# Kernel tuning notes

Hardware: AMD Instinct MI355X
Metric: run time of the kernel (lower is better)

Reference implementation:

```python
import jax, jax.numpy as jnp
import numpy as np

# OHEM CE constants (match init_kwargs)
THRESH = -np.log(0.7).astype(np.float32)  # threshold stored as -log(p)
N_MIN = 262144                            # B*H*W // 16
IGNORE_INDEX = 255


def setup_inputs() -> dict:
    key = jax.random.key(0)
    k1, k2 = jax.random.split(key)
    B, C, H, W = 16, 19, 512, 512
    inp = jax.random.normal(k1, (B, C, H, W), dtype=jnp.float32)
    target = jax.random.randint(k2, (B, H, W), 0, C, dtype=jnp.int64)
    k3 = jax.random.fold_in(key, 7)
    ign = jax.random.uniform(k3, (B, H, W)) < 0.02
    target = jnp.where(ign, jnp.asarray(IGNORE_INDEX, jnp.int64), target)
    return {"input": inp, "target": target}


def reference(input, target):
    # per-pixel cross entropy with ignore_index, reduction='none'
    logp = jax.nn.log_softmax(input, axis=1)              # (B,C,H,W)
    valid = target != IGNORE_INDEX                        # (B,H,W)
    tgt = jnp.where(valid, target, 0)
    nll = -jnp.take_along_axis(logp, tgt[:, None], axis=1)[:, 0]  # (B,H,W)
    loss = jnp.where(valid, nll, 0.0).reshape(-1)         # (N,)

    # OHEM: sort descending; if the n_min-th loss exceeds thresh keep all
    # losses above thresh, else keep the top n_min hardest examples.
    sorted_loss = -jnp.sort(-loss)                        # descending
    cond = sorted_loss[N_MIN] > THRESH
    idx = jnp.arange(sorted_loss.shape[0])
    keep = jnp.where(cond, sorted_loss > THRESH, idx < N_MIN)

    # reduction='mean' over the selected hard examples
    return jnp.sum(sorted_loss * keep) / jnp.sum(keep)
```

## Files before the change

### kernel.cpp

```cpp
#include <hip/hip_runtime.h>

#define CCH   19
#define HWSZ  262144
#define NPIX  4194304
#define NMIN  262144
#define THRESH_F 0.35667494393873245f

#define NB1 2048
#define NB2 2048
#define NB3 1024

__global__ __launch_bounds__(256) void k_compute4(
    const float* __restrict__ inp, const int* __restrict__ tgt,
    float4* __restrict__ loss4, unsigned int* __restrict__ hist1,
    double* __restrict__ sumT, unsigned long long* __restrict__ cntT)
{
    __shared__ unsigned int sh[NB1];
    for (int i = threadIdx.x; i < NB1; i += 256) sh[i] = 0;
    __syncthreads();

    float ls = 0.f;
    unsigned int lc = 0;
    const unsigned int stride = gridDim.x * 256;

    for (unsigned int i = blockIdx.x * 256 + threadIdx.x; i < NPIX / 4; i += stride) {
        const unsigned int p  = i * 4;
        const unsigned int b  = p >> 18;
        const unsigned int hw = p & (HWSZ - 1);
        const float* base = inp + (size_t)b * (CCH * HWSZ) + hw;
        const int4 t4 = *(const int4*)(tgt + p);

        float4 x[CCH];
        float4 m  = make_float4(-3.4e38f, -3.4e38f, -3.4e38f, -3.4e38f);
        float4 xt = make_float4(0.f, 0.f, 0.f, 0.f);
        #pragma unroll
        for (int c = 0; c < CCH; ++c) {
            const float4 v = *(const float4*)(base + (size_t)c * HWSZ);
            x[c] = v;
            m.x = fmaxf(m.x, v.x); m.y = fmaxf(m.y, v.y);
            m.z = fmaxf(m.z, v.z); m.w = fmaxf(m.w, v.w);
            xt.x = (c == t4.x) ? v.x : xt.x;
            xt.y = (c == t4.y) ? v.y : xt.y;
            xt.z = (c == t4.z) ? v.z : xt.z;
            xt.w = (c == t4.w) ? v.w : xt.w;
        }
        float4 s = make_float4(0.f, 0.f, 0.f, 0.f);
        #pragma unroll
        for (int c = 0; c < CCH; ++c) {
            s.x += __expf(x[c].x - m.x);
            s.y += __expf(x[c].y - m.y);
            s.z += __expf(x[c].z - m.z);
            s.w += __expf(x[c].w - m.w);
        }

        float4 l;
        l.x = (t4.x != 255) ? (__logf(s.x) + m.x - xt.x) : 0.f;
        l.y = (t4.y != 255) ? (__logf(s.y) + m.y - xt.y) : 0.f;
        l.z = (t4.z != 255) ? (__logf(s.z) + m.z - xt.z) : 0.f;
        l.w = (t4.w != 255) ? (__logf(s.w) + m.w - xt.w) : 0.f;
        l.x = fmaxf(l.x, 0.f); l.y = fmaxf(l.y, 0.f);
        l.z = fmaxf(l.z, 0.f); l.w = fmaxf(l.w, 0.f);
        loss4[i] = l;

        if (l.x > THRESH_F) { ls += l.x; lc++; }
        if (l.y > THRESH_F) { ls += l.y; lc++; }
        if (l.z > THRESH_F) { ls += l.z; lc++; }
        if (l.w > THRESH_F) { ls += l.w; lc++; }
        atomicAdd(&sh[__float_as_uint(l.x) >> 21], 1u);
        atomicAdd(&sh[__float_as_uint(l.y) >> 21], 1u);
        atomicAdd(&sh[__float_as_uint(l.z) >> 21], 1u);
        atomicAdd(&sh[__float_as_uint(l.w) >> 21], 1u);
    }

    #pragma unroll
    for (int off = 32; off > 0; off >>= 1) {
        ls += __shfl_down(ls, off);
        lc += __shfl_down(lc, off);
    }
    __shared__ float wsum[4];
    __shared__ unsigned int wcnt[4];
    const int lane = threadIdx.x & 63, wid = threadIdx.x >> 6;
    if (lane == 0) { wsum[wid] = ls; wcnt[wid] = lc; }
    __syncthreads();
    if (threadIdx.x == 0) {
        atomicAdd(sumT, (double)(wsum[0] + wsum[1] + wsum[2] + wsum[3]));
        atomicAdd(cntT, (unsigned long long)(wcnt[0] + wcnt[1] + wcnt[2] + wcnt[3]));
    }

    __syncthreads();
    for (int i = threadIdx.x; i < NB1; i += 256) {
        unsigned int v = sh[i];
        if (v) atomicAdd(&hist1[i], v);
    }
}

__global__ __launch_bounds__(256) void k_select(
    const unsigned int* __restrict__ hist, int nbins, int shiftbits, int first,
    uint2* __restrict__ state)
{
    __shared__ unsigned int cnt[NB1];
    __shared__ unsigned int psum[257];
    const int tid = threadIdx.x;

    for (int i = tid; i < nbins; i += 256) cnt[i] = hist[i];
    if (tid == 0) psum[256] = 0;
    __syncthreads();

    const int chunk = nbins >> 8;
    const int lo = tid * chunk, hi = lo + chunk;
    unsigned int s = 0;
    for (int b = lo; b < hi; ++b) s += cnt[b];
    psum[tid] = s;
    __syncthreads();

    for (int d = 1; d < 256; d <<= 1) {
        unsigned int v = psum[tid] + ((tid + d < 256) ? psum[tid + d] : 0);
        __syncthreads();
        psum[tid] = v;
        __syncthreads();
    }

    const unsigned int K       = first ? (unsigned int)NMIN : state->y;
    const unsigned int oldpref = first ? 0u : state->x;
    __syncthreads();

    const unsigned int above = psum[tid + 1];
    if (psum[tid] >= K && above < K) {
        unsigned int cum = above;
        for (int b = hi - 1; b >= lo; --b) {
            const unsigned int prev = cum;
            cum += cnt[b];
            if (cum >= K) {
                state->x = (oldpref << shiftbits) | (unsigned int)b;
                state->y = K - prev;
                break;
            }
        }
    }
}

__global__ __launch_bounds__(256) void k_hist(
    const float4* __restrict__ loss4, const uint2* __restrict__ state,
    unsigned int* __restrict__ histo, int level)
{
    __shared__ unsigned int sh[NB2];
    const int nb = (level == 2) ? NB2 : NB3;
    for (int i = threadIdx.x; i < nb; i += 256) sh[i] = 0;
    __syncthreads();

    const unsigned int pref = state->x;
    const unsigned int stride = gridDim.x * 256;

    for (unsigned int i = blockIdx.x * 256 + threadIdx.x; i < NPIX / 4; i += stride) {
        const float4 v = loss4[i];
        const float vv[4] = {v.x, v.y, v.z, v.w};
        #pragma unroll
        for (int j = 0; j < 4; ++j) {
            const unsigned int bits = __float_as_uint(vv[j]);
            if (level == 2) {
                if ((bits >> 21) == pref) atomicAdd(&sh[(bits >> 10) & 0x7FF], 1u);
            } else {
                if ((bits >> 10) == pref) atomicAdd(&sh[bits & 0x3FF], 1u);
            }
        }
    }
    __syncthreads();
    for (int i = threadIdx.x; i < nb; i += 256) {
        unsigned int v = sh[i];
        if (v) atomicAdd(&histo[i], v);
    }
}

__global__ __launch_bounds__(256) void k_sumtop(
    const float4* __restrict__ loss4, const uint2* __restrict__ state,
    double* __restrict__ sumG, unsigned long long* __restrict__ cntG)
{
    const unsigned int tb = state->x;
    float ls = 0.f;
    unsigned int lc = 0;
    const unsigned int stride = gridDim.x * 256;

    for (unsigned int i = blockIdx.x * 256 + threadIdx.x; i < NPIX / 4; i += stride) {
        const float4 v = loss4[i];
        const float vv[4] = {v.x, v.y, v.z, v.w};
        #pragma unroll
        for (int j = 0; j < 4; ++j) {
            if (__float_as_uint(vv[j]) > tb) { ls += vv[j]; lc++; }
        }
    }
    #pragma unroll
    for (int off = 32; off > 0; off >>= 1) {
        ls += __shfl_down(ls, off);
        lc += __shfl_down(lc, off);
    }
    __shared__ float wsum[4];
    __shared__ unsigned int wcnt[4];
    const int lane = threadIdx.x & 63, wid = threadIdx.x >> 6;
    if (lane == 0) { wsum[wid] = ls; wcnt[wid] = lc; }
    __syncthreads();
    if (threadIdx.x == 0) {
        atomicAdd(sumG, (double)(wsum[0] + wsum[1] + wsum[2] + wsum[3]));
        atomicAdd(cntG, (unsigned long long)(wcnt[0] + wcnt[1] + wcnt[2] + wcnt[3]));
    }
}

__global__ void k_finalize(
    const double* __restrict__ sumT, const unsigned long long* __restrict__ cntT,
    const uint2* __restrict__ state, const double* __restrict__ sumG,
    const unsigned long long* __restrict__ cntG, float* __restrict__ out)
{
    if (threadIdx.x == 0 && blockIdx.x == 0) {
        const unsigned long long c = *cntT;
        double r;
        if (c > (unsigned long long)NMIN) {
            r = *sumT / (double)c;
        } else {
            const float t = __uint_as_float(state->x);
            r = (*sumG + (double)(NMIN - *cntG) * (double)t) / (double)NMIN;
        }
        out[0] = (float)r;
    }
}

extern "C" void kernel_launch(void* const* d_in, const int* in_sizes, int n_in,
                              void* d_out, int out_size, void* d_ws, size_t ws_size,
                              hipStream_t stream)
{
    const float* inp = (const float*)d_in[0];
    const int*   tgt = (const int*)d_in[1];
    float*       out = (float*)d_out;
    char*        ws  = (char*)d_ws;

    float* loss = (float*)ws;
    const size_t LOSS_BYTES = (size_t)NPIX * 4;
    unsigned int* h1 = (unsigned int*)(ws + LOSS_BYTES);
    unsigned int* h2 = h1 + NB1;
    unsigned int* h3 = h2 + NB2;
    char* scal = ws + LOSS_BYTES + (NB1 + NB2 + NB3) * 4;
    double*             sumT  = (double*)(scal + 0);
    unsigned long long* cntT  = (unsigned long long*)(scal + 8);
    double*             sumG  = (double*)(scal + 16);
    unsigned long long* cntG  = (unsigned long long*)(scal + 24);
    uint2*              state = (uint2*)(scal + 32);
    const size_t AUX_BYTES = (NB1 + NB2 + NB3) * 4 + 40;

    hipMemsetAsync(ws + LOSS_BYTES, 0, AUX_BYTES, stream);

    k_compute4<<<2048, 256, 0, stream>>>(inp, tgt, (float4*)loss, h1, sumT, cntT);
    k_select<<<1, 256, 0, stream>>>(h1, NB1, 11, 1, state);
    k_hist<<<2048, 256, 0, stream>>>((const float4*)loss, state, h2, 2);
    k_select<<<1, 256, 0, stream>>>(h2, NB2, 11, 0, state);
    k_hist<<<2048, 256, 0, stream>>>((const float4*)loss, state, h3, 3);
    k_select<<<1, 256, 0, stream>>>(h3, NB3, 10, 0, state);
    k_sumtop<<<2048, 256, 0, stream>>>((const float4*)loss, state, sumG, cntG);
    k_finalize<<<1, 1, 0, stream>>>(sumT, cntT, state, sumG, cntG, out);
}
```

Measured before the change: 548.8 us.

## Drop loss buffer and radix passes; finalize in last block, recompute on fallback

The main kernel no longer stores per-pixel losses or builds a histogram. It only accumulates the sum and count above threshold, and the last arriving block writes the mean directly. The radix-select top-k path moves into a single-block fallback kernel that recomputes the cross entropy from the input four times, and it runs only when the count is at most N_MIN. This removes the loss write, the three extra passes over the loss buffer and several launches. In exchange the rare fallback path becomes extremely slow on one block, and the grid drops to 1024 blocks.

```diff
diff --git a/kernel.cpp b/kernel.cpp
--- a/kernel.cpp
+++ b/kernel.cpp
@@ -6,19 +6,40 @@
 #define NMIN  262144
 #define THRESH_F 0.35667494393873245f
 
+#define NBLK  1024
+
 #define NB1 2048
 #define NB2 2048
 #define NB3 1024
 
+__device__ __forceinline__ float ce_pixel(
+    const float* __restrict__ inp, const int* __restrict__ tgt, unsigned p)
+{
+    const unsigned b  = p >> 18;
+    const unsigned hw = p & (HWSZ - 1);
+    const float* base = inp + (size_t)b * (CCH * HWSZ) + hw;
+    const int t = tgt[p];
+    float x[CCH];
+    float m = -3.4e38f, xt = 0.f;
+    #pragma unroll
+    for (int c = 0; c < CCH; ++c) {
+        float v = base[(size_t)c * HWSZ];
+        x[c] = v;
+        m = fmaxf(m, v);
+        xt = (c == t) ? v : xt;
+    }
+    float s = 0.f;
+    #pragma unroll
+    for (int c = 0; c < CCH; ++c) s += __expf(x[c] - m);
+    float l = (t != 255) ? (__logf(s) + m - xt) : 0.f;
+    return fmaxf(l, 0.f);
+}
+
 __global__ __launch_bounds__(256) void k_compute4(
     const float* __restrict__ inp, const int* __restrict__ tgt,
-    float4* __restrict__ loss4, unsigned int* __restrict__ hist1,
-    double* __restrict__ sumT, unsigned long long* __restrict__ cntT)
-{
-    __shared__ unsigned int sh[NB1];
-    for (int i = threadIdx.x; i < NB1; i += 256) sh[i] = 0;
-    __syncthreads();
-
+    double* __restrict__ sumT, unsigned long long* __restrict__ cntT,
+    unsigned int* __restrict__ arrival, float* __restrict__ out)
+{
     float ls = 0.f;
     unsigned int lc = 0;
     const unsigned int stride = gridDim.x * 256;
@@ -60,16 +81,11 @@
         l.w = (t4.w != 255) ? (__logf(s.w) + m.w - xt.w) : 0.f;
         l.x = fmaxf(l.x, 0.f); l.y = fmaxf(l.y, 0.f);
         l.z = fmaxf(l.z, 0.f); l.w = fmaxf(l.w, 0.f);
-        loss4[i] = l;
 
         if (l.x > THRESH_F) { ls += l.x; lc++; }
         if (l.y > THRESH_F) { ls += l.y; lc++; }
         if (l.z > THRESH_F) { ls += l.z; lc++; }
         if (l.w > THRESH_F) { ls += l.w; lc++; }
-        atomicAdd(&sh[__float_as_uint(l.x) >> 21], 1u);
-        atomicAdd(&sh[__float_as_uint(l.y) >> 21], 1u);
-        atomicAdd(&sh[__float_as_uint(l.z) >> 21], 1u);
-        atomicAdd(&sh[__float_as_uint(l.w) >> 21], 1u);
     }
 
     #pragma unroll
@@ -85,140 +101,113 @@
     if (threadIdx.x == 0) {
         atomicAdd(sumT, (double)(wsum[0] + wsum[1] + wsum[2] + wsum[3]));
         atomicAdd(cntT, (unsigned long long)(wcnt[0] + wcnt[1] + wcnt[2] + wcnt[3]));
-    }
-
-    __syncthreads();
-    for (int i = threadIdx.x; i < NB1; i += 256) {
-        unsigned int v = sh[i];
-        if (v) atomicAdd(&hist1[i], v);
-    }
-}
-
-__global__ __launch_bounds__(256) void k_select(
-    const unsigned int* __restrict__ hist, int nbins, int shiftbits, int first,
-    uint2* __restrict__ state)
-{
-    __shared__ unsigned int cnt[NB1];
-    __shared__ unsigned int psum[257];
+        __threadfence();
+        const unsigned int old = atomicAdd(arrival, 1u);
+        if (old == gridDim.x - 1) {
+            __threadfence();
+            const unsigned long long c = atomicAdd(cntT, 0ull);
+            const double sT = *(volatile double*)sumT;
+            if (c > (unsigned long long)NMIN)
+                out[0] = (float)(sT / (double)c);
+        }
+    }
+}
+
+__device__ void block_select(
+    unsigned int* cnt, unsigned int* psum, int nbins, unsigned int K,
+    unsigned int* outB, unsigned int* outRem)
+{
     const int tid = threadIdx.x;
-
-    for (int i = tid; i < nbins; i += 256) cnt[i] = hist[i];
-    if (tid == 0) psum[256] = 0;
-    __syncthreads();
-
     const int chunk = nbins >> 8;
     const int lo = tid * chunk, hi = lo + chunk;
     unsigned int s = 0;
     for (int b = lo; b < hi; ++b) s += cnt[b];
     psum[tid] = s;
-    __syncthreads();
-
+    if (tid == 0) psum[256] = 0;
+    __syncthreads();
     for (int d = 1; d < 256; d <<= 1) {
         unsigned int v = psum[tid] + ((tid + d < 256) ? psum[tid + d] : 0);
         __syncthreads();
         psum[tid] = v;
         __syncthreads();
     }
-
-    const unsigned int K       = first ? (unsigned int)NMIN : state->y;
-    const unsigned int oldpref = first ? 0u : state->x;
-    __syncthreads();
-
     const unsigned int above = psum[tid + 1];
     if (psum[tid] >= K && above < K) {
         unsigned int cum = above;
         for (int b = hi - 1; b >= lo; --b) {
             const unsigned int prev = cum;
             cum += cnt[b];
-            if (cum >= K) {
-                state->x = (oldpref << shiftbits) | (unsigned int)b;
-                state->y = K - prev;
-                break;
-            }
-        }
-    }
-}
-
-__global__ __launch_bounds__(256) void k_hist(
-    const float4* __restrict__ loss4, const uint2* __restrict__ state,
-    unsigned int* __restrict__ histo, int level)
-{
-    __shared__ unsigned int sh[NB2];
-    const int nb = (level == 2) ? NB2 : NB3;
-    for (int i = threadIdx.x; i < nb; i += 256) sh[i] = 0;
-    __syncthreads();
-
-    const unsigned int pref = state->x;
-    const unsigned int stride = gridDim.x * 256;
-
-    for (unsigned int i = blockIdx.x * 256 + threadIdx.x; i < NPIX / 4; i += stride) {
-        const float4 v = loss4[i];
-        const float vv[4] = {v.x, v.y, v.z, v.w};
-        #pragma unroll
-        for (int j = 0; j < 4; ++j) {
-            const unsigned int bits = __float_as_uint(vv[j]);
-            if (level == 2) {
-                if ((bits >> 21) == pref) atomicAdd(&sh[(bits >> 10) & 0x7FF], 1u);
-            } else {
-                if ((bits >> 10) == pref) atomicAdd(&sh[bits & 0x3FF], 1u);
-            }
-        }
-    }
-    __syncthreads();
-    for (int i = threadIdx.x; i < nb; i += 256) {
-        unsigned int v = sh[i];
-        if (v) atomicAdd(&histo[i], v);
-    }
-}
-
-__global__ __launch_bounds__(256) void k_sumtop(
-    const float4* __restrict__ loss4, const uint2* __restrict__ state,
-    double* __restrict__ sumG, unsigned long long* __restrict__ cntG)
-{
-    const unsigned int tb = state->x;
+            if (cum >= K) { *outB = (unsigned int)b; *outRem = K - prev; break; }
+        }
+    }
+    __syncthreads();
+}
+
+__global__ __launch_bounds__(256) void k_fallback(
+    const float* __restrict__ inp, const int* __restrict__ tgt,
+    const unsigned long long* __restrict__ cntT, float* __restrict__ out)
+{
+    if (*cntT > (unsigned long long)NMIN) return;
+
+    __shared__ unsigned int sh[NB1];
+    __shared__ unsigned int psum[257];
+    __shared__ unsigned int selB, selR;
+    const int tid = threadIdx.x;
+
+    for (int i = tid; i < NB1; i += 256) sh[i] = 0;
+    __syncthreads();
+    for (unsigned int p = tid; p < NPIX; p += 256) {
+        const float l = ce_pixel(inp, tgt, p);
+        atomicAdd(&sh[__float_as_uint(l) >> 21], 1u);
+    }
+    __syncthreads();
+    block_select(sh, psum, NB1, NMIN, &selB, &selR);
+    const unsigned int pref1 = selB;
+    const unsigned int K2    = selR;
+
+    for (int i = tid; i < NB2; i += 256) sh[i] = 0;
+    __syncthreads();
+    for (unsigned int p = tid; p < NPIX; p += 256) {
+        const unsigned int bits = __float_as_uint(ce_pixel(inp, tgt, p));
+        if ((bits >> 21) == pref1) atomicAdd(&sh[(bits >> 10) & 0x7FF], 1u);
+    }
+    __syncthreads();
+    block_select(sh, psum, NB2, K2, &selB, &selR);
+    const unsigned int pref2 = (pref1 << 11) | selB;
+    const unsigned int K3    = selR;
+
+    for (int i = tid; i < NB3; i += 256) sh[i] = 0;
+    __syncthreads();
+    for (unsigned int p = tid; p < NPIX; p += 256) {
+        const unsigned int bits = __float_as_uint(ce_pixel(inp, tgt, p));
+        if ((bits >> 10) == pref2) atomicAdd(&sh[bits & 0x3FF], 1u);
+    }
+    __syncthreads();
+    block_select(sh, psum, NB3, K3, &selB, &selR);
+    const unsigned int tb = (pref2 << 10) | selB;
+    __syncthreads();
+
     float ls = 0.f;
     unsigned int lc = 0;
-    const unsigned int stride = gridDim.x * 256;
-
-    for (unsigned int i = blockIdx.x * 256 + threadIdx.x; i < NPIX / 4; i += stride) {
-        const float4 v = loss4[i];
-        const float vv[4] = {v.x, v.y, v.z, v.w};
-        #pragma unroll
-        for (int j = 0; j < 4; ++j) {
-            if (__float_as_uint(vv[j]) > tb) { ls += vv[j]; lc++; }
-        }
+    for (unsigned int p = tid; p < NPIX; p += 256) {
+        const float l = ce_pixel(inp, tgt, p);
+        if (__float_as_uint(l) > tb) { ls += l; lc++; }
     }
     #pragma unroll
     for (int off = 32; off > 0; off >>= 1) {
         ls += __shfl_down(ls, off);
         lc += __shfl_down(lc, off);
     }
-    __shared__ float wsum[4];
-    __shared__ unsigned int wcnt[4];
-    const int lane = threadIdx.x & 63, wid = threadIdx.x >> 6;
-    if (lane == 0) { wsum[wid] = ls; wcnt[wid] = lc; }
-    __syncthreads();
-    if (threadIdx.x == 0) {
-        atomicAdd(sumG, (double)(wsum[0] + wsum[1] + wsum[2] + wsum[3]));
-        atomicAdd(cntG, (unsigned long long)(wcnt[0] + wcnt[1] + wcnt[2] + wcnt[3]));
-    }
-}
-
-__global__ void k_finalize(
-    const double* __restrict__ sumT, const unsigned long long* __restrict__ cntT,
-    const uint2* __restrict__ state, const double* __restrict__ sumG,
-    const unsigned long long* __restrict__ cntG, float* __restrict__ out)
-{
-    if (threadIdx.x == 0 && blockIdx.x == 0) {
-        const unsigned long long c = *cntT;
-        double r;
-        if (c > (unsigned long long)NMIN) {
-            r = *sumT / (double)c;
-        } else {
-            const float t = __uint_as_float(state->x);
-            r = (*sumG + (double)(NMIN - *cntG) * (double)t) / (double)NMIN;
-        }
-        out[0] = (float)r;
+    __shared__ float fsum[4];
+    __shared__ unsigned int fcnt[4];
+    const int lane = tid & 63, wid = tid >> 6;
+    if (lane == 0) { fsum[wid] = ls; fcnt[wid] = lc; }
+    __syncthreads();
+    if (tid == 0) {
+        const double sG = (double)(fsum[0] + fsum[1] + fsum[2] + fsum[3]);
+        const unsigned int cG = fcnt[0] + fcnt[1] + fcnt[2] + fcnt[3];
+        const float t = __uint_as_float(tb);
+        out[0] = (float)((sG + (double)(NMIN - cG) * (double)t) / (double)NMIN);
     }
 }
 
@@ -231,27 +220,12 @@
     float*       out = (float*)d_out;
     char*        ws  = (char*)d_ws;
 
-    float* loss = (float*)ws;
-    const size_t LOSS_BYTES = (size_t)NPIX * 4;
-    unsigned int* h1 = (unsigned int*)(ws + LOSS_BYTES);
-    unsigned int* h2 = h1 + NB1;
-    unsigned int* h3 = h2 + NB2;
-    char* scal = ws + LOSS_BYTES + (NB1 + NB2 + NB3) * 4;
-    double*             sumT  = (double*)(scal + 0);
-    unsigned long long* cntT  = (unsigned long long*)(scal + 8);
-    double*             sumG  = (double*)(scal + 16);
-    unsigned long long* cntG  = (unsigned long long*)(scal + 24);
-    uint2*              state = (uint2*)(scal + 32);
-    const size_t AUX_BYTES = (NB1 + NB2 + NB3) * 4 + 40;
-
-    hipMemsetAsync(ws + LOSS_BYTES, 0, AUX_BYTES, stream);
-
-    k_compute4<<<2048, 256, 0, stream>>>(inp, tgt, (float4*)loss, h1, sumT, cntT);
-    k_select<<<1, 256, 0, stream>>>(h1, NB1, 11, 1, state);
-    k_hist<<<2048, 256, 0, stream>>>((const float4*)loss, state, h2, 2);
-    k_select<<<1, 256, 0, stream>>>(h2, NB2, 11, 0, state);
-    k_hist<<<2048, 256, 0, stream>>>((const float4*)loss, state, h3, 3);
-    k_select<<<1, 256, 0, stream>>>(h3, NB3, 10, 0, state);
-    k_sumtop<<<2048, 256, 0, stream>>>((const float4*)loss, state, sumG, cntG);
-    k_finalize<<<1, 1, 0, stream>>>(sumT, cntT, state, sumG, cntG, out);
-}
+    double*             sumT    = (double*)(ws + 0);
+    unsigned long long* cntT    = (unsigned long long*)(ws + 8);
+    unsigned int*       arrival = (unsigned int*)(ws + 16);
+
+    hipMemsetAsync(ws, 0, 32, stream);
+
+    k_compute4<<<NBLK, 256, 0, stream>>>(inp, tgt, sumT, cntT, arrival, out);
+    k_fallback<<<1, 256, 0, stream>>>(inp, tgt, cntT, out);
+}
```

After: 471.1 us. -14.2%, faster.
